# Optimization experiments

Measured on AMD Instinct MI355X. Metric: run time of the kernel, lower is better.

The kernel has to match this reference:

```python
import jax, jax.numpy as jnp
import numpy as np
import math

B, N, M, O = 64, 2048, 64, 128  # batch, neurons, in_dims, out_dims


def setup_inputs() -> dict:
    key = jax.random.key(0)
    kx, kw, kb = jax.random.split(key, 3)
    s = 1.0 / math.sqrt(M + O)
    x = jax.random.normal(kx, (B, N, M), dtype=jnp.float32)
    # master weights fp32, init U(-s, s) as in the torch module
    w1 = jax.random.uniform(kw, (M, O, N), dtype=jnp.float32, minval=-s, maxval=s)
    b1 = jnp.zeros((1, N, O), dtype=jnp.float32)
    return {"x": x, "w1": w1, "b1": b1}


def reference(x, w1, b1):
    # N independent per-neuron linears: [B,N,M] x [M,O,N] -> [B,N,O]
    # cast master weights/bias to compute dtype (matches .to(x.dtype))
    w = w1.astype(x.dtype)
    b = b1.astype(x.dtype)
    return jnp.einsum('bnm,mon->bno', x, w) + b
```

## Files before the change

### kernel.cpp

```cpp
#include <hip/hip_runtime.h>
#include <hip/hip_bf16.h>

#define B_DIM 64
#define N_TOT 2048
#define M_DIM 64
#define O_DIM 128
#define NT 8

typedef __bf16 bf16x8 __attribute__((ext_vector_type(8)));
typedef float f32x4 __attribute__((ext_vector_type(4)));

__device__ __forceinline__ unsigned short f2bf(float f) {
    union { float f; unsigned int u; } v;
    v.f = f;
    unsigned int r = v.u + 0x7fffu + ((v.u >> 16) & 1u);
    return (unsigned short)(r >> 16);
}

__global__ __launch_bounds__(512, 2) void superlinear_mfma(
    const float* __restrict__ x, const float* __restrict__ w1,
    const float* __restrict__ b1, float* __restrict__ out)
{
    __shared__ unsigned char wlds[NT * O_DIM * M_DIM * 2];

    const int tid  = threadIdx.x;
    const int lane = tid & 63;
    const int wave = tid >> 6;

    const int bid  = blockIdx.x;
    const int nblk = (bid & 7) * 32 + (bid >> 3);
    const int n0   = nblk * NT;

    #pragma unroll
    for (int it = 0; it < 8; ++it) {
        int u  = it * 512 + tid;
        int n4 = u & 1;
        int o  = (u >> 1) & 127;
        int mq = u >> 8;
        int m  = mq * 4;
        const float* gp = w1 + ((size_t)m * O_DIM + o) * N_TOT + n0 + n4 * 4;
        float4 r0 = *(const float4*)(gp);
        float4 r1 = *(const float4*)(gp + (size_t)O_DIM * N_TOT);
        float4 r2 = *(const float4*)(gp + (size_t)2 * O_DIM * N_TOT);
        float4 r3 = *(const float4*)(gp + (size_t)3 * O_DIM * N_TOT);
        const float* a0 = (const float*)&r0;
        const float* a1 = (const float*)&r1;
        const float* a2 = (const float*)&r2;
        const float* a3 = (const float*)&r3;
        #pragma unroll
        for (int j = 0; j < 4; ++j) {
            int nn = n4 * 4 + j;
            unsigned short e0 = f2bf(a0[j]);
            unsigned short e1 = f2bf(a1[j]);
            unsigned short e2 = f2bf(a2[j]);
            unsigned short e3 = f2bf(a3[j]);
            unsigned long long pk =
                (unsigned long long)e0 | ((unsigned long long)e1 << 16) |
                ((unsigned long long)e2 << 32) | ((unsigned long long)e3 << 48);
            unsigned addr = (unsigned)(nn * (O_DIM * M_DIM * 2) + o * (M_DIM * 2) + m * 2);
            addr ^= (unsigned)((o & 7) << 4);
            *(unsigned long long*)(wlds + addr) = pk;
        }
    }
    __syncthreads();

    const int nn  = wave;
    const int n   = n0 + nn;
    const int col = lane & 15;
    const int kg  = lane >> 4;

    f32x4 acc[4][8];
    #pragma unroll
    for (int ot = 0; ot < 8; ++ot) {
        float bv = b1[(size_t)n * O_DIM + ot * 16 + col];
        #pragma unroll
        for (int bt = 0; bt < 4; ++bt) {
            acc[bt][ot][0] = bv; acc[bt][ot][1] = bv;
            acc[bt][ot][2] = bv; acc[bt][ot][3] = bv;
        }
    }

    #pragma unroll
    for (int kc = 0; kc < 2; ++kc) {
        bf16x8 af[4];
        #pragma unroll
        for (int bt = 0; bt < 4; ++bt) {
            int b = bt * 16 + col;
            const float* xp = x + ((size_t)b * N_TOT + n) * M_DIM + kc * 32 + kg * 8;
            float4 lo = *(const float4*)xp;
            float4 hi = *(const float4*)(xp + 4);
            const float* lp = (const float*)&lo;
            const float* hp = (const float*)&hi;
            union { bf16x8 v; unsigned short s[8]; } cvt;
            #pragma unroll
            for (int j = 0; j < 4; ++j) { cvt.s[j] = f2bf(lp[j]); cvt.s[4 + j] = f2bf(hp[j]); }
            af[bt] = cvt.v;
        }
        #pragma unroll
        for (int ot = 0; ot < 8; ++ot) {
            unsigned addr = (unsigned)(nn * 16384 + (ot * 16 + col) * 128 + kc * 64 + kg * 16);
            addr ^= (unsigned)((col & 7) << 4);
            bf16x8 bfrag = *(const bf16x8*)(wlds + addr);
            #pragma unroll
            for (int bt = 0; bt < 4; ++bt)
                acc[bt][ot] = __builtin_amdgcn_mfma_f32_16x16x32_bf16(af[bt], bfrag, acc[bt][ot], 0, 0, 0);
        }
    }

    #pragma unroll
    for (int bt = 0; bt < 4; ++bt) {
        #pragma unroll
        for (int r = 0; r < 4; ++r) {
            int b = bt * 16 + kg * 4 + r;
            float* op = out + ((size_t)b * N_TOT + n) * O_DIM + col;
            #pragma unroll
            for (int ot = 0; ot < 8; ++ot)
                op[ot * 16] = acc[bt][ot][r];
        }
    }
}

extern "C" void kernel_launch(void* const* d_in, const int* in_sizes, int n_in,
                              void* d_out, int out_size, void* d_ws, size_t ws_size,
                              hipStream_t stream) {
    const float* x  = (const float*)d_in[0];
    const float* w1 = (const float*)d_in[1];
    const float* b1 = (const float*)d_in[2];
    float* out = (float*)d_out;
    superlinear_mfma<<<dim3(256), dim3(512), 0, stream>>>(x, w1, b1, out);
}
```

Before: 35.55 us.

## Split batch across twice the waves, prefetch x before weight staging, stream outputs

Doubles the block to 1024 threads so each wave handles half the batch for one neuron, which cuts per-wave accumulator registers. Loads of x and bias are issued before the weight staging and __syncthreads so their latency overlaps the LDS fill. Hand-rolled bf16 rounding is replaced with native __bf16 casts. Output is computed per output tile, with the two K chunks chained in MFMA, and written with nontemporal stores. The cost is a larger block, which may limit how many blocks fit per CU, and more LDS-read traffic per MFMA.

After: 40.14 us. 1.13x slower.

```diff
diff --git a/kernel.cpp b/kernel.cpp
--- a/kernel.cpp
+++ b/kernel.cpp
@@ -1,23 +1,16 @@
 #include <hip/hip_runtime.h>
 #include <hip/hip_bf16.h>
 
-#define B_DIM 64
 #define N_TOT 2048
 #define M_DIM 64
 #define O_DIM 128
 #define NT 8
 
 typedef __bf16 bf16x8 __attribute__((ext_vector_type(8)));
+typedef __bf16 bf16x4 __attribute__((ext_vector_type(4)));
 typedef float f32x4 __attribute__((ext_vector_type(4)));
 
-__device__ __forceinline__ unsigned short f2bf(float f) {
-    union { float f; unsigned int u; } v;
-    v.f = f;
-    unsigned int r = v.u + 0x7fffu + ((v.u >> 16) & 1u);
-    return (unsigned short)(r >> 16);
-}
-
-__global__ __launch_bounds__(512, 2) void superlinear_mfma(
+__global__ __launch_bounds__(1024, 4) void superlinear_mfma(
     const float* __restrict__ x, const float* __restrict__ w1,
     const float* __restrict__ b1, float* __restrict__ out)
 {
@@ -31,9 +24,31 @@
     const int nblk = (bid & 7) * 32 + (bid >> 3);
     const int n0   = nblk * NT;
 
+    const int nn  = wave & 7;
+    const int bh  = wave >> 3;
+    const int n   = n0 + nn;
+    const int col = lane & 15;
+    const int kg  = lane >> 4;
+
+    float4 xr[2][2][2];
     #pragma unroll
-    for (int it = 0; it < 8; ++it) {
-        int u  = it * 512 + tid;
+    for (int kc = 0; kc < 2; ++kc) {
+        #pragma unroll
+        for (int bt = 0; bt < 2; ++bt) {
+            int b = bh * 32 + bt * 16 + col;
+            const float* xp = x + ((size_t)b * N_TOT + n) * M_DIM + kc * 32 + kg * 8;
+            xr[kc][bt][0] = *(const float4*)xp;
+            xr[kc][bt][1] = *(const float4*)(xp + 4);
+        }
+    }
+    float bv[8];
+    #pragma unroll
+    for (int ot = 0; ot < 8; ++ot)
+        bv[ot] = b1[(size_t)n * O_DIM + ot * 16 + col];
+
+    #pragma unroll
+    for (int it = 0; it < 4; ++it) {
+        int u  = it * 1024 + tid;
         int n4 = u & 1;
         int o  = (u >> 1) & 127;
         int mq = u >> 8;
@@ -49,73 +64,55 @@
         const float* a3 = (const float*)&r3;
         #pragma unroll
         for (int j = 0; j < 4; ++j) {
-            int nn = n4 * 4 + j;
-            unsigned short e0 = f2bf(a0[j]);
-            unsigned short e1 = f2bf(a1[j]);
-            unsigned short e2 = f2bf(a2[j]);
-            unsigned short e3 = f2bf(a3[j]);
-            unsigned long long pk =
-                (unsigned long long)e0 | ((unsigned long long)e1 << 16) |
-                ((unsigned long long)e2 << 32) | ((unsigned long long)e3 << 48);
-            unsigned addr = (unsigned)(nn * (O_DIM * M_DIM * 2) + o * (M_DIM * 2) + m * 2);
+            int nnw = n4 * 4 + j;
+            bf16x4 pk;
+            pk[0] = (__bf16)a0[j];
+            pk[1] = (__bf16)a1[j];
+            pk[2] = (__bf16)a2[j];
+            pk[3] = (__bf16)a3[j];
+            unsigned addr = (unsigned)(nnw * 16384 + o * 128 + m * 2);
             addr ^= (unsigned)((o & 7) << 4);
-            *(unsigned long long*)(wlds + addr) = pk;
-        }
-    }
-    __syncthreads();
-
-    const int nn  = wave;
-    const int n   = n0 + nn;
-    const int col = lane & 15;
-    const int kg  = lane >> 4;
-
-    f32x4 acc[4][8];
-    #pragma unroll
-    for (int ot = 0; ot < 8; ++ot) {
-        float bv = b1[(size_t)n * O_DIM + ot * 16 + col];
-        #pragma unroll
-        for (int bt = 0; bt < 4; ++bt) {
-            acc[bt][ot][0] = bv; acc[bt][ot][1] = bv;
-            acc[bt][ot][2] = bv; acc[bt][ot][3] = bv;
+            *(bf16x4*)(wlds + addr) = pk;
         }
     }
 
+    bf16x8 af[2][2];
     #pragma unroll
     for (int kc = 0; kc < 2; ++kc) {
-        bf16x8 af[4];
         #pragma unroll
-        for (int bt = 0; bt < 4; ++bt) {
-            int b = bt * 16 + col;
-            const float* xp = x + ((size_t)b * N_TOT + n) * M_DIM + kc * 32 + kg * 8;
-            float4 lo = *(const float4*)xp;
-            float4 hi = *(const float4*)(xp + 4);
-            const float* lp = (const float*)&lo;
-            const float* hp = (const float*)&hi;
-            union { bf16x8 v; unsigned short s[8]; } cvt;
+        for (int bt = 0; bt < 2; ++bt) {
+            const float* lp = (const float*)&xr[kc][bt][0];
+            const float* hp = (const float*)&xr[kc][bt][1];
+            bf16x8 v;
             #pragma unroll
-            for (int j = 0; j < 4; ++j) { cvt.s[j] = f2bf(lp[j]); cvt.s[4 + j] = f2bf(hp[j]); }
-            af[bt] = cvt.v;
-        }
-        #pragma unroll
-        for (int ot = 0; ot < 8; ++ot) {
-            unsigned addr = (unsigned)(nn * 16384 + (ot * 16 + col) * 128 + kc * 64 + kg * 16);
-            addr ^= (unsigned)((col & 7) << 4);
-            bf16x8 bfrag = *(const bf16x8*)(wlds + addr);
-            #pragma unroll
-            for (int bt = 0; bt < 4; ++bt)
-                acc[bt][ot] = __builtin_amdgcn_mfma_f32_16x16x32_bf16(af[bt], bfrag, acc[bt][ot], 0, 0, 0);
+            for (int j = 0; j < 4; ++j) {
+                v[j]     = (__bf16)lp[j];
+                v[4 + j] = (__bf16)hp[j];
+            }
+            af[kc][bt] = v;
         }
     }
 
+    __syncthreads();
+
     #pragma unroll
-    for (int bt = 0; bt < 4; ++bt) {
+    for (int ot = 0; ot < 8; ++ot) {
+        unsigned addr = (unsigned)(nn * 16384 + (ot * 16 + col) * 128 + kg * 16);
+        addr ^= (unsigned)((col & 7) << 4);
+        bf16x8 bf0 = *(const bf16x8*)(wlds + addr);
+        bf16x8 bf1 = *(const bf16x8*)(wlds + (addr ^ 64u));
+        f32x4 ci;
+        ci[0] = bv[ot]; ci[1] = bv[ot]; ci[2] = bv[ot]; ci[3] = bv[ot];
         #pragma unroll
-        for (int r = 0; r < 4; ++r) {
-            int b = bt * 16 + kg * 4 + r;
-            float* op = out + ((size_t)b * N_TOT + n) * O_DIM + col;
+        for (int bt = 0; bt < 2; ++bt) {
+            f32x4 a = __builtin_amdgcn_mfma_f32_16x16x32_bf16(af[0][bt], bf0, ci, 0, 0, 0);
+            a       = __builtin_amdgcn_mfma_f32_16x16x32_bf16(af[1][bt], bf1, a,  0, 0, 0);
             #pragma unroll
-            for (int ot = 0; ot < 8; ++ot)
-                op[ot * 16] = acc[bt][ot][r];
+            for (int r = 0; r < 4; ++r) {
+                int b = bh * 32 + bt * 16 + kg * 4 + r;
+                __builtin_nontemporal_store(
+                    a[r], out + ((size_t)b * N_TOT + n) * O_DIM + ot * 16 + col);
+            }
         }
     }
 }
@@ -127,5 +124,5 @@
     const float* w1 = (const float*)d_in[1];
     const float* b1 = (const float*)d_in[2];
     float* out = (float*)d_out;
-    superlinear_mfma<<<dim3(256), dim3(512), 0, stream>>>(x, w1, b1, out);
+    superlinear_mfma<<<dim3(256), dim3(1024), 0, stream>>>(x, w1, b1, out);
 }
```
